# Kernel tuning notes

Hardware: AMD Instinct MI355X
Metric: run time of the kernel (lower is better)

## Reference

```python
import jax, jax.numpy as jnp
import numpy as np

B, S, IN, H, OUT = 64, 512, 1024, 512, 512
EPS = 1e-5
ADAPTIVE_RATE = 0.01


def setup_inputs() -> dict:
    key = jax.random.key(0)
    ks = iter(jax.random.split(key, 64))

    def rn(shape, scale):
        return (jax.random.normal(next(ks), shape, jnp.float32) * scale)

    d = {}
    d["x"] = jax.random.normal(next(ks), (B, S, IN), jnp.float32)
    d["context"] = jax.random.normal(next(ks), (B, H), jnp.float32)
    d["state_importance"] = jnp.ones((1, H), jnp.float32)
    # embedding
    d["W_emb"], d["b_emb"] = rn((H, IN), 0.02), rn((H,), 0.01)
    # core layers: Linear + BatchNorm1d (gamma=1, beta=0 torch init)
    d["W0"], d["b0"] = rn((H, H), 0.03), rn((H,), 0.01)
    d["g0"], d["bt0"] = jnp.ones((H,), jnp.float32), jnp.zeros((H,), jnp.float32)
    d["W1"], d["b1"] = rn((H, H), 0.03), rn((H,), 0.01)
    d["g1"], d["bt1"] = jnp.ones((H,), jnp.float32), jnp.zeros((H,), jnp.float32)
    # two LSTMCells (hidden -> hidden), torch gate order i,f,g,o
    lstm_scale = 1.0 / np.sqrt(H)
    for l in range(2):
        d[f"Wih{l}"] = rn((4 * H, H), lstm_scale)
        d[f"Whh{l}"] = rn((4 * H, H), lstm_scale)
        d[f"bih{l}"] = rn((4 * H,), lstm_scale)
        d[f"bhh{l}"] = rn((4 * H,), lstm_scale)
    # compression gate: Linear(2H, H) + LayerNorm + Sigmoid
    d["Wc"], d["bc"] = rn((H, 2 * H), 0.02), rn((H,), 0.01)
    d["lnc_g"], d["lnc_b"] = jnp.ones((H,), jnp.float32), jnp.zeros((H,), jnp.float32)
    # importance generator: Linear, ReLU, Linear, LayerNorm, Sigmoid
    d["Wi1"], d["bi1"] = rn((H, H), 0.03), rn((H,), 0.01)
    d["Wi2"], d["bi2"] = rn((H, H), 0.03), rn((H,), 0.01)
    d["lni_g"], d["lni_b"] = jnp.ones((H,), jnp.float32), jnp.zeros((H,), jnp.float32)
    # final layer
    d["Wf"], d["bf"] = rn((OUT, H), 0.03), rn((OUT,), 0.01)
    return d


def _bn_channel_dim1(h, gamma, beta):
    # BatchNorm1d (training mode) on (B, S, H) with channel dim = dim 1 (S == num_features)
    m = h.mean(axis=(0, 2), keepdims=True)
    v = h.var(axis=(0, 2), keepdims=True)  # biased, like torch normalization
    return gamma[None, :, None] * (h - m) / jnp.sqrt(v + EPS) + beta[None, :, None]


def _ln(h, g, b):
    m = h.mean(-1, keepdims=True)
    v = h.var(-1, keepdims=True)
    return g * (h - m) / jnp.sqrt(v + EPS) + b


def _lstm_cell(xt, h, c, Wih, Whh, bih, bhh):
    z = xt @ Wih.T + bih + h @ Whh.T + bhh  # (B, 4H)
    i, f, g, o = jnp.split(z, 4, axis=-1)
    c = jax.nn.sigmoid(f) * c + jax.nn.sigmoid(i) * jnp.tanh(g)
    h = jax.nn.sigmoid(o) * jnp.tanh(c)
    return h, c


def reference(x, context, state_importance, W_emb, b_emb,
              W0, b0, g0, bt0, W1, b1, g1, bt1,
              Wih0, Whh0, bih0, bhh0, Wih1, Whh1, bih1, bhh1,
              Wc, bc, lnc_g, lnc_b, Wi1, bi1, Wi2, bi2, lni_g, lni_b,
              Wf, bf):
    h = x @ W_emb.T + b_emb  # (B, S, H)
    h = jax.nn.relu(_bn_channel_dim1(h @ W0.T + b0, g0, bt0))
    h = jax.nn.relu(_bn_channel_dim1(h @ W1.T + b1, g1, bt1))

    # stacked 2-layer LSTMCell over the sequence, keep only the final hidden
    zeros = jnp.zeros((B, H), h.dtype)

    def step(carry, xt):
        h0, c0, h1, c1 = carry
        h0, c0 = _lstm_cell(xt, h0, c0, Wih0, Whh0, bih0, bhh0)
        h1, c1 = _lstm_cell(h0, h1, c1, Wih1, Whh1, bih1, bhh1)
        return (h0, c0, h1, c1), None

    (h0, c0, h1, c1), _ = jax.lax.scan(step, (zeros, zeros, zeros, zeros),
                                       jnp.swapaxes(h, 0, 1))
    processed = h1  # (B, H)

    comp = jax.nn.sigmoid(_ln(jnp.concatenate([processed, context], axis=-1) @ Wc.T + bc,
                              lnc_g, lnc_b))
    compressed = processed * comp

    imp = jax.nn.sigmoid(_ln(jax.nn.relu(compressed @ Wi1.T + bi1) @ Wi2.T + bi2,
                             lni_g, lni_b))
    si_new = state_importance + ADAPTIVE_RATE * (
        jnp.abs(imp).mean(axis=0, keepdims=True) - state_importance)

    out = compressed @ Wf.T + bf
    return out, si_new
```

## Files before the change

### kernel.cpp

```cpp
#include <hip/hip_runtime.h>
#include <hip/hip_bf16.h>
#include <stdint.h>


typedef __attribute__((ext_vector_type(8))) short short8;
typedef __attribute__((ext_vector_type(4))) float floatx4;
typedef __attribute__((ext_vector_type(4))) unsigned uintx4;

__device__ inline float b2f(short u){
  union { float f; uint32_t i; } x; x.i = ((uint32_t)(uint16_t)u) << 16; return x.f;
}
__device__ inline short f2b(float f){
  union { float f; uint32_t i; } x; x.f = f;
  uint32_t r = (x.i + 0x7FFFu + ((x.i >> 16) & 1u)) >> 16;
  return (short)(uint16_t)r;
}
__device__ inline float sigm(float x){ return 1.0f / (1.0f + __expf(-x)); }

__device__ inline float blk_sum(float v, float* red){
  #pragma unroll
  for (int o = 32; o > 0; o >>= 1) v += __shfl_down(v, o, 64);
  int wv = threadIdx.x >> 6;
  __syncthreads();
  if ((threadIdx.x & 63) == 0) red[wv] = v;
  __syncthreads();
  return red[0] + red[1] + red[2] + red[3];
}

__device__ inline void stage16(const short* g, short* l){
  __builtin_amdgcn_global_load_lds(
      (const __attribute__((address_space(1))) void*)(uintptr_t)g,
      (__attribute__((address_space(3))) void*)(uintptr_t)l,
      16, 0, 0);
}


__global__ void set_flag(const unsigned* __restrict__ si_bits, unsigned* __restrict__ flag){
  if (threadIdx.x == 0 && blockIdx.x == 0)
    *flag = (si_bits[0] == 0x3F800000u) ? 1u : 0u;
}


__global__ __launch_bounds__(256) void convq(
    const unsigned* __restrict__ flag, int mode,
    const void* s0, long e0, short* d0, int n0,
    const void* s1, long e1, short* d1, int n1,
    const void* s2, long e2, short* d2, int n2,
    const void* s3, long e3, short* d3, int n3)
{
  const bool isf32 = (*flag != 0u);
  const int gid = blockIdx.x*256 + threadIdx.x;
  const int stride = gridDim.x*256;
  const void* ss[4] = {s0,s1,s2,s3};
  long ee[4]  = {e0,e1,e2,e3};
  short* dd[4] = {d0,d1,d2,d3};
  int nn[4]   = {n0,n1,n2,n3};
  for (int s = 0; s < 4; s++){
    if (!dd[s]) continue;
    if (mode == 1) {
      if (!isf32) continue;
      for (int i = gid; i < nn[s]; i += stride)
        dd[s][i] = ((const short*)ss[s])[ee[s] + i];
    } else if (isf32) {
      for (int i = gid; i < nn[s]; i += stride)
        dd[s][i] = f2b(((const float*)ss[s])[ee[s] + i]);
    } else {
      for (int i = gid; i < nn[s]; i += stride)
        dd[s][i] = ((const short*)ss[s])[ee[s] + i];
    }
  }
}


__global__ __launch_bounds__(256) void gemm_bt(
    const short* __restrict__ A, const short* __restrict__ A2, int splitRow,
    int lda, const short* __restrict__ W, const short* __restrict__ bias,
    short* __restrict__ C, int ldc, int row0, int K)
{
  __shared__ alignas(16) short As[128*32];
  __shared__ alignas(16) short Bs[128*32];
  const int tid  = threadIdx.x;
  const int lane = tid & 63;
  const int wave = tid >> 6;
  const int wm = wave >> 1, wn = wave & 1;
  const int bm = blockIdx.x, bn = blockIdx.y;
  const int R0 = row0 + bm*128;
  const short* Ab = (R0 < splitRow) ? A2 : A;

  floatx4 acc[4][4];
  #pragma unroll
  for (int i = 0; i < 4; i++)
    #pragma unroll
    for (int j = 0; j < 4; j++){ floatx4 z = {0.f,0.f,0.f,0.f}; acc[i][j] = z; }

  const short* Ag = Ab + (size_t)(R0 + (tid >> 2))*lda + (tid & 3)*8;
  const short* Wg = W  + (size_t)(bn*128 + (tid >> 2))*K + (tid & 3)*8;

  const int kk  = (lane >> 4) * 8;
  const int rA  = wm*64 + (lane & 15);
  const int rB  = wn*64 + (lane & 15);

  for (int k0 = 0; k0 < K; k0 += 32) {
    __syncthreads();
    stage16(Ag + k0,                  As + tid*8);
    stage16(Ag + k0 + (size_t)64*lda, As + 2048 + tid*8);
    stage16(Wg + k0,                  Bs + tid*8);
    stage16(Wg + k0 + (size_t)64*K,   Bs + 2048 + tid*8);
    __syncthreads();

    short8 af[4], bf[4];
    #pragma unroll
    for (int i = 0; i < 4; i++){
      af[i] = *(const short8*)&As[(rA + i*16)*32 + kk];
      bf[i] = *(const short8*)&Bs[(rB + i*16)*32 + kk];
    }
    #pragma unroll
    for (int i = 0; i < 4; i++)
      #pragma unroll
      for (int j = 0; j < 4; j++)
        acc[i][j] = __builtin_amdgcn_mfma_f32_16x16x32_bf16(af[i], bf[j], acc[i][j], 0, 0, 0);
  }

  const int crow0 = R0 + wm*64 + (lane >> 4)*4;
  const int ccol0 = bn*128 + wn*64;
  #pragma unroll
  for (int i = 0; i < 4; i++){
    #pragma unroll
    for (int j = 0; j < 4; j++){
      int col = ccol0 + j*16 + (lane & 15);
      float bv = b2f(bias[col]);
      #pragma unroll
      for (int r = 0; r < 4; r++){
        int row = crow0 + i*16 + r;
        C[(size_t)row*ldc + col] = f2b(acc[i][j][r] + bv);
      }
    }
  }
}


__global__ __launch_bounds__(256) void bn_relu(
    const short* __restrict__ X, const short* __restrict__ gamma,
    const short* __restrict__ beta, short* __restrict__ Y)
{
  const int s = blockIdx.x, tid = threadIdx.x;
  __shared__ float red[4];
  float s1 = 0.f, s2 = 0.f;
  for (int i = tid; i < 4096; i += 256){
    int b = i >> 6, c = i & 63;
    short8 v = *(const short8*)(X + ((size_t)(b*512 + s))*512 + c*8);
    #pragma unroll
    for (int u = 0; u < 8; u++){ float f = b2f(v[u]); s1 += f; s2 += f*f; }
  }
  s1 = blk_sum(s1, red);
  s2 = blk_sum(s2, red);
  float mean = s1 * (1.f/32768.f);
  float var  = fmaxf(s2 * (1.f/32768.f) - mean*mean, 0.f);
  float sc = b2f(gamma[s]) * rsqrtf(var + 1e-5f);
  float sh = b2f(beta[s]) - mean * sc;
  for (int i = tid; i < 4096; i += 256){
    int b = i >> 6, c = i & 63;
    size_t base = ((size_t)(b*512 + s))*512 + c*8;
    short8 v = *(const short8*)(X + base);
    short8 o;
    #pragma unroll
    for (int u = 0; u < 8; u++){
      float f = b2f(v[u]) * sc + sh;
      o[u] = f2b(fmaxf(f, 0.f));
    }
    *(short8*)(Y + base) = o;
  }
}


__global__ __launch_bounds__(256, 1) void lstm_persist(
    const short* __restrict__ Xseq,
    const short* __restrict__ Wih0, const short* __restrict__ Whh0,
    const short* __restrict__ bih0, const short* __restrict__ bhh0,
    const short* __restrict__ Wih1, const short* __restrict__ Whh1,
    const short* __restrict__ bih1, const short* __restrict__ bhh1,
    short* __restrict__ h0r,
    short* __restrict__ h1r,
    unsigned* __restrict__ slots)
{
  const int wg   = blockIdx.x;
  const int tid  = threadIdx.x;
  const int lane = tid & 63;
  const int wave = tid >> 6;
  const int l15  = lane & 15;
  const int quad = lane >> 4;
  const int kq   = quad * 8;

  __shared__ float zp[4*64*33];
  __shared__ unsigned pack[2][256];
  #define ZP(t,r,c) zp[((t)*64 + (r))*33 + (c)]

  const short* Wt = (wave==0) ? Wih0 : (wave==1) ? Whh0 : (wave==2) ? Wih1 : Whh1;
  short8 wreg[2][16];
  #pragma unroll
  for (int nt = 0; nt < 2; nt++){
    int g2 = nt*2 + (l15 >> 3);
    int ml = l15 & 7;
    const short* wrow = Wt + (size_t)(g2*512 + wg*8 + ml)*512 + kq;
    #pragma unroll
    for (int kk = 0; kk < 16; kk++)
      wreg[nt][kk] = *(const short8*)(wrow + kk*32);
  }

  const int bb  = tid >> 2;
  const int ml0 = (tid & 3) * 2;
  float bs0[4][2], bs1[4][2];
  #pragma unroll
  for (int g = 0; g < 4; g++)
    #pragma unroll
    for (int p = 0; p < 2; p++){
      int m = wg*8 + ml0 + p;
      bs0[g][p] = b2f(bih0[g*512+m]) + b2f(bhh0[g*512+m]);
      bs1[g][p] = b2f(bih1[g*512+m]) + b2f(bhh1[g*512+m]);
    }
  float c0[2] = {0.f, 0.f}, c1[2] = {0.f, 0.f};

  for (int it = 0; it <= 512; ++it){
    const bool act = (wave==0) ? (it < 512)
                   : (wave==1) ? (it >= 1 && it < 512)
                   : (wave==2) ? (it >= 1)
                   :             (it >= 2);

    if (it > 0 && wave > 0 && act){
      const unsigned want = (unsigned)it;
      const unsigned* sp = slots + lane*16;
      for (;;){
        unsigned v;
        asm volatile("global_load_dword %0, %1, off sc1\n\t"
                     "s_waitcnt vmcnt(0)"
                     : "=v"(v) : "v"(sp) : "memory");
        if (__all((int)(v >= want))) break;
      }
      __builtin_amdgcn_sched_barrier(0);
    }

    floatx4 acc[4][2];
    #pragma unroll
    for (int mt = 0; mt < 4; mt++)
      #pragma unroll
      for (int nt = 0; nt < 2; nt++){ floatx4 z = {0.f,0.f,0.f,0.f}; acc[mt][nt] = z; }

    if (act){
      const short* Ab;
      size_t rstride;
      if (wave == 0)      { Ab = Xseq + (size_t)it*512;               rstride = 262144; }
      else if (wave <= 2) { Ab = h0r + (size_t)((it-1)&1)*32768;      rstride = 512; }
      else                { Ab = h1r + (size_t)(it&1)*32768;          rstride = 512; }
      const short* ap[4];
      #pragma unroll
      for (int mt = 0; mt < 4; mt++)
        ap[mt] = Ab + (size_t)(mt*16 + l15)*rstride + kq;

      if (wave == 0){
        #pragma unroll
        for (int kk = 0; kk < 16; kk++){
          short8 af[4];
          #pragma unroll
          for (int mt = 0; mt < 4; mt++) af[mt] = *(const short8*)(ap[mt] + kk*32);
          #pragma unroll
          for (int mt = 0; mt < 4; mt++){
            acc[mt][0] = __builtin_amdgcn_mfma_f32_16x16x32_bf16(af[mt], wreg[0][kk], acc[mt][0], 0, 0, 0);
            acc[mt][1] = __builtin_amdgcn_mfma_f32_16x16x32_bf16(af[mt], wreg[1][kk], acc[mt][1], 0, 0, 0);
          }
        }
      } else {
        short8 hb[2][4][4];
        #pragma unroll
        for (int pb = 0; pb < 2; pb++)
          #pragma unroll
          for (int kk = 0; kk < 4; kk++)
            #pragma unroll
            for (int mt = 0; mt < 4; mt++)
              asm volatile("global_load_dwordx4 %0, %1, off sc1"
                           : "=v"(hb[pb][kk][mt])
                           : "v"(ap[mt] + (pb*4 + kk)*32));
        #pragma unroll
        for (int kb = 0; kb < 4; kb++){
          const int cur = kb & 1;
          if (kb < 3) asm volatile("s_waitcnt vmcnt(16)" ::: "memory");
          else        asm volatile("s_waitcnt vmcnt(0)"  ::: "memory");
          __builtin_amdgcn_sched_barrier(0);
          #pragma unroll
          for (int kk = 0; kk < 4; kk++)
            #pragma unroll
            for (int mt = 0; mt < 4; mt++){
              acc[mt][0] = __builtin_amdgcn_mfma_f32_16x16x32_bf16(hb[cur][kk][mt], wreg[0][kb*4+kk], acc[mt][0], 0, 0, 0);
              acc[mt][1] = __builtin_amdgcn_mfma_f32_16x16x32_bf16(hb[cur][kk][mt], wreg[1][kb*4+kk], acc[mt][1], 0, 0, 0);
            }
          if (kb < 2){
            #pragma unroll
            for (int kk = 0; kk < 4; kk++)
              #pragma unroll
              for (int mt = 0; mt < 4; mt++)
                asm volatile("global_load_dwordx4 %0, %1, off sc1"
                             : "=v"(hb[cur][kk][mt])
                             : "v"(ap[mt] + ((kb+2)*4 + kk)*32));
          }
        }
      }
    }

    #pragma unroll
    for (int mt = 0; mt < 4; mt++)
      #pragma unroll
      for (int nt = 0; nt < 2; nt++)
        #pragma unroll
        for (int r = 0; r < 4; r++)
          ZP(wave, mt*16 + quad*4 + r, nt*16 + l15) = acc[mt][nt][r];
    __syncthreads();

    if (it < 512){
      float hv[2];
      #pragma unroll
      for (int p = 0; p < 2; p++){
        int ml = ml0 + p;
        float zi = ZP(0, bb,      ml) + ZP(1, bb,      ml) + bs0[0][p];
        float zf = ZP(0, bb,  8 + ml) + ZP(1, bb,  8 + ml) + bs0[1][p];
        float zg = ZP(0, bb, 16 + ml) + ZP(1, bb, 16 + ml) + bs0[2][p];
        float zo = ZP(0, bb, 24 + ml) + ZP(1, bb, 24 + ml) + bs0[3][p];
        c0[p] = sigm(zf)*c0[p] + sigm(zi)*tanhf(zg);
        hv[p] = sigm(zo)*tanhf(c0[p]);
      }
      pack[0][tid] = (unsigned)(uint16_t)f2b(hv[0]) | ((unsigned)(uint16_t)f2b(hv[1]) << 16);
    }
    if (it >= 1){
      float hv[2];
      #pragma unroll
      for (int p = 0; p < 2; p++){
        int ml = ml0 + p;
        float zi = ZP(2, bb,      ml) + ZP(3, bb,      ml) + bs1[0][p];
        float zf = ZP(2, bb,  8 + ml) + ZP(3, bb,  8 + ml) + bs1[1][p];
        float zg = ZP(2, bb, 16 + ml) + ZP(3, bb, 16 + ml) + bs1[2][p];
        float zo = ZP(2, bb, 24 + ml) + ZP(3, bb, 24 + ml) + bs1[3][p];
        c1[p] = sigm(zf)*c1[p] + sigm(zi)*tanhf(zg);
        hv[p] = sigm(zo)*tanhf(c1[p]);
      }
      pack[1][tid] = (unsigned)(uint16_t)f2b(hv[0]) | ((unsigned)(uint16_t)f2b(hv[1]) << 16);
    }
    __syncthreads();

    if (wave == 0 && it < 512){
      uintx4 d = *(const uintx4*)&pack[0][lane*4];
      short* dst = h0r + (size_t)(it&1)*32768 + lane*512 + wg*8;
      asm volatile("global_store_dwordx4 %0, %1, off sc0 sc1" :: "v"(dst), "v"(d) : "memory");
      asm volatile("s_waitcnt vmcnt(0)" ::: "memory");
    }
    if (wave == 1 && it >= 1){
      uintx4 d = *(const uintx4*)&pack[1][lane*4];
      short* dst = h1r + (size_t)((it-1)&1)*32768 + lane*512 + wg*8;
      asm volatile("global_store_dwordx4 %0, %1, off sc0 sc1" :: "v"(dst), "v"(d) : "memory");
      asm volatile("s_waitcnt vmcnt(0)" ::: "memory");
    }
    __syncthreads();
    if (tid == 0){
      unsigned nv = (unsigned)(it + 1);
      asm volatile("global_store_dword %0, %1, off sc0 sc1"
                   :: "v"(slots + wg*16), "v"(nv) : "memory");
    }
  }
  #undef ZP
}


__global__ __launch_bounds__(256) void head_gate_out(
    const short* __restrict__ h1, const short* __restrict__ ctx,
    const short* __restrict__ Wc, const short* __restrict__ bc,
    const short* __restrict__ lng, const short* __restrict__ lnb,
    const short* __restrict__ Wf, const short* __restrict__ bfb,
    short* __restrict__ compressed, void* __restrict__ outp,
    const unsigned* __restrict__ flag)
{
  const int b = blockIdx.x, tid = threadIdx.x;
  const bool isf32 = (*flag != 0u);
  __shared__ float xc[1024];
  __shared__ float cv[512];
  __shared__ float red[4];
  for (int i = tid; i < 512; i += 256) xc[i]       = b2f(h1 [b*512 + i]);
  for (int i = tid; i < 512; i += 256) xc[512 + i] = b2f(ctx[b*512 + i]);
  __syncthreads();
  float y[2];
  #pragma unroll
  for (int jj = 0; jj < 2; jj++){
    int j = tid + jj*256;
    const short* wr = Wc + (size_t)j*1024;
    float a = 0.f;
    for (int k = 0; k < 1024; k += 8){
      short8 wv = *(const short8*)(wr + k);
      #pragma unroll
      for (int u = 0; u < 8; u++) a += b2f(wv[u]) * xc[k + u];
    }
    y[jj] = a + b2f(bc[j]);
  }
  float s = blk_sum(y[0] + y[1], red);
  float mean = s * (1.f/512.f);
  float q = (y[0]-mean)*(y[0]-mean) + (y[1]-mean)*(y[1]-mean);
  q = blk_sum(q, red);
  float inv = rsqrtf(q * (1.f/512.f) + 1e-5f);
  #pragma unroll
  for (int jj = 0; jj < 2; jj++){
    int j = tid + jj*256;
    float v = (y[jj]-mean)*inv*b2f(lng[j]) + b2f(lnb[j]);
    float cm = xc[j] * sigm(v);
    cv[j] = cm;
    compressed[(size_t)b*512 + j] = f2b(cm);
  }
  __syncthreads();
  #pragma unroll
  for (int jj = 0; jj < 2; jj++){
    int j = tid + jj*256;
    const short* wr = Wf + (size_t)j*512;
    float a = 0.f;
    for (int k = 0; k < 512; k += 8){
      short8 wv = *(const short8*)(wr + k);
      #pragma unroll
      for (int u = 0; u < 8; u++) a += b2f(wv[u]) * cv[k + u];
    }
    float o = a + b2f(bfb[j]);
    if (isf32) ((float*)outp)[(size_t)b*512 + j] = o;
    else       ((short*)outp)[(size_t)b*512 + j] = f2b(o);
  }
}


__global__ __launch_bounds__(256) void head_imp(
    const short* __restrict__ compressed,
    const short* __restrict__ Wi1, const short* __restrict__ bi1,
    const short* __restrict__ Wi2, const short* __restrict__ bi2,
    const short* __restrict__ lng, const short* __restrict__ lnb,
    float* __restrict__ imp)
{
  const int b = blockIdx.x, tid = threadIdx.x;
  __shared__ float xr[512];
  __shared__ float t1[512];
  __shared__ float red[4];
  for (int i = tid; i < 512; i += 256) xr[i] = b2f(compressed[b*512 + i]);
  __syncthreads();
  #pragma unroll
  for (int jj = 0; jj < 2; jj++){
    int j = tid + jj*256;
    const short* wr = Wi1 + (size_t)j*512;
    float a = 0.f;
    for (int k = 0; k < 512; k += 8){
      short8 wv = *(const short8*)(wr + k);
      #pragma unroll
      for (int u = 0; u < 8; u++) a += b2f(wv[u]) * xr[k + u];
    }
    t1[j] = fmaxf(a + b2f(bi1[j]), 0.f);
  }
  __syncthreads();
  float y[2];
  #pragma unroll
  for (int jj = 0; jj < 2; jj++){
    int j = tid + jj*256;
    const short* wr = Wi2 + (size_t)j*512;
    float a = 0.f;
    for (int k = 0; k < 512; k += 8){
      short8 wv = *(const short8*)(wr + k);
      #pragma unroll
      for (int u = 0; u < 8; u++) a += b2f(wv[u]) * t1[k + u];
    }
    y[jj] = a + b2f(bi2[j]);
  }
  float s = blk_sum(y[0] + y[1], red);
  float mean = s * (1.f/512.f);
  float q = (y[0]-mean)*(y[0]-mean) + (y[1]-mean)*(y[1]-mean);
  q = blk_sum(q, red);
  float inv = rsqrtf(q * (1.f/512.f) + 1e-5f);
  #pragma unroll
  for (int jj = 0; jj < 2; jj++){
    int j = tid + jj*256;
    imp[(size_t)b*512 + j] = sigm((y[jj]-mean)*inv*b2f(lng[j]) + b2f(lnb[j]));
  }
}


__global__ __launch_bounds__(256) void head_si(
    const float* __restrict__ imp, const short* __restrict__ si,
    void* __restrict__ outp, const unsigned* __restrict__ flag)
{
  int tid = threadIdx.x;
  const bool isf32 = (*flag != 0u);
  #pragma unroll
  for (int mm = 0; mm < 2; mm++){
    int m = tid + mm*256;
    float s = 0.f;
    for (int b = 0; b < 64; b++) s += fabsf(imp[(size_t)b*512 + m]);
    float mean = s * (1.f/64.f);
    float sv = b2f(si[m]);
    float o = sv + 0.01f*(mean - sv);
    if (isf32) ((float*)outp)[32768 + m] = o;
    else       ((short*)outp)[32768 + m] = f2b(o);
  }
}


extern "C" void kernel_launch(void* const* d_in, const int* in_sizes, int n_in,
                              void* d_out, int out_size, void* d_ws, size_t ws_size,
                              hipStream_t stream)
{
  (void)in_sizes; (void)n_in; (void)out_size; (void)ws_size;
  char* ws = (char*)d_ws;
  unsigned* slots  = (unsigned*)(ws);
  unsigned* flag   = (unsigned*)(ws + 4096);
  short*    xStage = (short*)(ws + 8192);
  short*    ring   = (short*)(ws + 270336);
  short*    comp   = (short*)(ws + 925696);
  float*    impb   = (float*)(ws + 991232);
  short*    SA     = (short*)(ws + 1122304);

  short* h0r = ring;
  short* h1r = ring + 65536;

  short* aWemb = SA + 0;
  short* aW0   = SA + 524288;
  short* aW1   = SA + 786432;
  short* aWih0 = SA + 1048576;
  short* aWhh0 = SA + 2097152;
  short* aWih1 = SA + 3145728;
  short* aWhh1 = SA + 4194304;
  short* aWc   = SA + 5242880;
  short* aWi1  = SA + 5767168;
  short* aWi2  = SA + 6029312;
  short* aWf   = SA + 6291456;
  short* V     = SA + 6553600;
  short* abemb = V + 0;     short* ab0  = V + 512;   short* ag0  = V + 1024;
  short* abt0  = V + 1536;  short* ab1  = V + 2048;  short* ag1  = V + 2560;
  short* abt1  = V + 3072;  short* abih0= V + 3584;  short* abhh0= V + 5632;
  short* abih1 = V + 7680;  short* abhh1= V + 9728;  short* abc  = V + 11776;
  short* alncg = V + 12288; short* alncb= V + 12800; short* abi1 = V + 13312;
  short* abi2  = V + 13824; short* alnig= V + 14336; short* alnib= V + 14848;
  short* abfb  = V + 15360; short* actx = V + 15872; short* asi  = V + 48640;

  short* xb  = (short*)d_in[0];
  short* hL0 = xb + 16777216;

  hipMemsetAsync(slots, 0, 4096, stream);
  set_flag<<<1, 64, 0, stream>>>((const unsigned*)d_in[2], flag);

  dim3 blk(256);
  convq<<<256, blk, 0, stream>>>(flag, 0,
      d_in[0], 0, xStage, 65536, nullptr,0,nullptr,0, nullptr,0,nullptr,0, nullptr,0,nullptr,0);
  for (long n0 = 65536; n0 < 33554432; n0 <<= 1) {
    int blocks = (int)((n0 + 1023) / 1024); if (blocks > 4096) blocks = 4096;
    convq<<<blocks, blk, 0, stream>>>(flag, 0,
        d_in[0], n0, xb + n0, (int)n0, nullptr,0,nullptr,0, nullptr,0,nullptr,0, nullptr,0,nullptr,0);
  }
  convq<<<64, blk, 0, stream>>>(flag, 1,
      xStage, 0, xb, 65536, nullptr,0,nullptr,0, nullptr,0,nullptr,0, nullptr,0,nullptr,0);

  convq<<<1024, blk, 0, stream>>>(flag, 0,
      d_in[3], 0, aWemb, 524288,  d_in[5], 0, aW0, 262144,
      d_in[9], 0, aW1,   262144,  d_in[21],0, aWc, 524288);
  convq<<<2048, blk, 0, stream>>>(flag, 0,
      d_in[13],0, aWih0, 1048576, d_in[14],0, aWhh0, 1048576,
      d_in[17],0, aWih1, 1048576, d_in[18],0, aWhh1, 1048576);
  convq<<<1024, blk, 0, stream>>>(flag, 0,
      d_in[25],0, aWi1, 262144,   d_in[27],0, aWi2, 262144,
      d_in[31],0, aWf,  262144,   d_in[1], 0, actx, 32768);
  convq<<<8, blk, 0, stream>>>(flag, 0,
      d_in[4], 0, abemb, 512,  d_in[6], 0, ab0, 512,
      d_in[7], 0, ag0,   512,  d_in[8], 0, abt0, 512);
  convq<<<8, blk, 0, stream>>>(flag, 0,
      d_in[10],0, ab1, 512,  d_in[11],0, ag1, 512,
      d_in[12],0, abt1,512,  d_in[22],0, abc, 512);
  convq<<<8, blk, 0, stream>>>(flag, 0,
      d_in[15],0, abih0, 2048,  d_in[16],0, abhh0, 2048,
      d_in[19],0, abih1, 2048,  d_in[20],0, abhh1, 2048);
  convq<<<8, blk, 0, stream>>>(flag, 0,
      d_in[23],0, alncg, 512,  d_in[24],0, alncb, 512,
      d_in[26],0, abi1,  512,  d_in[28],0, abi2,  512);
  convq<<<8, blk, 0, stream>>>(flag, 0,
      d_in[29],0, alnig, 512,  d_in[30],0, alnib, 512,
      d_in[32],0, abfb,  512,  d_in[2], 0, asi,   512);

  gemm_bt<<<dim3(1, 4), blk, 0, stream>>>(xb, xb, 0, 1024, aWemb, abemb,
                                          xStage, 512, 0, 1024);
  for (int r0 = 128; r0 < 32768; r0 <<= 1) {
    gemm_bt<<<dim3(r0/128, 4), blk, 0, stream>>>(xb, xb, 0, 1024, aWemb, abemb,
                                                 xb, 512, r0, 1024);
  }
  gemm_bt<<<dim3(256, 4), blk, 0, stream>>>(xb, xStage, 128, 512, aW0, ab0,
                                            hL0, 512, 0, 512);
  bn_relu<<<512, blk, 0, stream>>>(hL0, ag0, abt0, hL0);
  gemm_bt<<<dim3(256, 4), blk, 0, stream>>>(hL0, hL0, 0, 512, aW1, ab1,
                                            xb, 512, 0, 512);
  bn_relu<<<512, blk, 0, stream>>>(xb, ag1, abt1, xb);

  lstm_persist<<<64, blk, 0, stream>>>(xb, aWih0, aWhh0, abih0, abhh0,
                                       aWih1, aWhh1, abih1, abhh1,
                                       h0r, h1r, slots);

  head_gate_out<<<64, blk, 0, stream>>>(h1r + 32768, actx, aWc, abc, alncg, alncb,
                                        aWf, abfb, comp, d_out, flag);
  head_imp<<<64, blk, 0, stream>>>(comp, aWi1, abi1, aWi2, abi2, alnig, alnib, impb);
  head_si<<<1, blk, 0, stream>>>(impb, asi, d_out, flag);
}
```

Measured before the change: 8.365 ms.

## Add aggregator block for LSTM grid barrier and prefetch future input rows

Adds a 65th workgroup that polls all 64 per-block progress slots and publishes a single epoch counter per block. Worker waves then spin on one word instead of each lane reading all 64 slots, which cuts polling traffic on the cross-block barrier. Wave 0 also stages the input rows for step it+2 into shared memory, warming the cache before they are needed. The extra hop through the aggregator adds latency to every step, and the prefetch adds load work on the critical wave.

```diff
diff --git a/kernel.cpp b/kernel.cpp
--- a/kernel.cpp
+++ b/kernel.cpp
@@ -181,18 +181,39 @@
     const short* __restrict__ bih1, const short* __restrict__ bhh1,
     short* __restrict__ h0r,
     short* __restrict__ h1r,
-    unsigned* __restrict__ slots)
+    unsigned* __restrict__ slots,
+    unsigned* __restrict__ epoch)
 {
   const int wg   = blockIdx.x;
   const int tid  = threadIdx.x;
   const int lane = tid & 63;
   const int wave = tid >> 6;
+
+  if (wg == 64){
+    if (wave != 0) return;
+    const unsigned* sp = slots + lane*16;
+    unsigned* ep = epoch + lane*16;
+    for (unsigned itv = 1; itv <= 512; ++itv){
+      for (;;){
+        unsigned v;
+        asm volatile("global_load_dword %0, %1, off sc1\n\t"
+                     "s_waitcnt vmcnt(0)"
+                     : "=v"(v) : "v"(sp) : "memory");
+        if (__all((int)(v >= itv))) break;
+      }
+      asm volatile("global_store_dword %0, %1, off sc0 sc1"
+                   :: "v"(ep), "v"(itv) : "memory");
+    }
+    return;
+  }
+
   const int l15  = lane & 15;
   const int quad = lane >> 4;
   const int kq   = quad * 8;
 
   __shared__ float zp[4*64*33];
   __shared__ unsigned pack[2][256];
+  __shared__ alignas(16) short xpf[512];
   #define ZP(t,r,c) zp[((t)*64 + (r))*33 + (c)]
 
   const short* Wt = (wave==0) ? Wih0 : (wave==1) ? Whh0 : (wave==2) ? Wih1 : Whh1;
@@ -228,13 +249,13 @@
 
     if (it > 0 && wave > 0 && act){
       const unsigned want = (unsigned)it;
-      const unsigned* sp = slots + lane*16;
+      const unsigned* ep = epoch + wg*16;
       for (;;){
         unsigned v;
         asm volatile("global_load_dword %0, %1, off sc1\n\t"
                      "s_waitcnt vmcnt(0)"
-                     : "=v"(v) : "v"(sp) : "memory");
-        if (__all((int)(v >= want))) break;
+                     : "=v"(v) : "v"(ep) : "memory");
+        if (v >= want) break;
       }
       __builtin_amdgcn_sched_barrier(0);
     }
@@ -362,6 +383,12 @@
       asm volatile("global_store_dword %0, %1, off sc0 sc1"
                    :: "v"(slots + wg*16), "v"(nv) : "memory");
     }
+    if (wave == 0 && it + 2 < 512){
+      const short* nx = Xseq + (size_t)(it + 2)*512 + lane*8;
+      #pragma unroll 8
+      for (int r = 0; r < 64; ++r)
+        stage16(nx + (size_t)r*262144, xpf);
+    }
   }
   #undef ZP
 }
@@ -506,12 +533,13 @@
   (void)in_sizes; (void)n_in; (void)out_size; (void)ws_size;
   char* ws = (char*)d_ws;
   unsigned* slots  = (unsigned*)(ws);
-  unsigned* flag   = (unsigned*)(ws + 4096);
-  short*    xStage = (short*)(ws + 8192);
-  short*    ring   = (short*)(ws + 270336);
-  short*    comp   = (short*)(ws + 925696);
-  float*    impb   = (float*)(ws + 991232);
-  short*    SA     = (short*)(ws + 1122304);
+  unsigned* epoch  = (unsigned*)(ws + 4096);
+  unsigned* flag   = (unsigned*)(ws + 8192);
+  short*    xStage = (short*)(ws + 12288);
+  short*    ring   = (short*)(ws + 274432);
+  short*    comp   = (short*)(ws + 798720);
+  float*    impb   = (float*)(ws + 864256);
+  short*    SA     = (short*)(ws + 995328);
 
   short* h0r = ring;
   short* h1r = ring + 65536;
@@ -539,7 +567,7 @@
   short* xb  = (short*)d_in[0];
   short* hL0 = xb + 16777216;
 
-  hipMemsetAsync(slots, 0, 4096, stream);
+  hipMemsetAsync(slots, 0, 8192, stream);
   set_flag<<<1, 64, 0, stream>>>((const unsigned*)d_in[2], flag);
 
   dim3 blk(256);
@@ -591,9 +619,9 @@
                                             xb, 512, 0, 512);
   bn_relu<<<512, blk, 0, stream>>>(xb, ag1, abt1, xb);
 
-  lstm_persist<<<64, blk, 0, stream>>>(xb, aWih0, aWhh0, abih0, abhh0,
+  lstm_persist<<<65, blk, 0, stream>>>(xb, aWih0, aWhh0, abih0, abhh0,
                                        aWih1, aWhh1, abih1, abhh1,
-                                       h0r, h1r, slots);
+                                       h0r, h1r, slots, epoch);
 
   head_gate_out<<<64, blk, 0, stream>>>(h1r + 32768, actx, aWc, abc, alncg, alncb,
                                         aWf, abfb, comp, d_out, flag);
```

Result: faster. 7.044 ms (-15.8%).
